# Kernel optimization log

Hardware: AMD Instinct MI355X
Metric: run time of the kernel (lower is better)

## Reference

```python
import jax, jax.numpy as jnp
import numpy as np

B, N, E, H = 2, 2048, 2048, 16
D = E // H  # head_dim = 128


def setup_inputs() -> dict:
    key = jax.random.key(0)
    k1, k2, k3, k4 = jax.random.split(key, 4)
    x = jax.random.normal(k1, (B, N, E), dtype=jnp.float32)
    Wq = jax.random.normal(k2, (E, E), dtype=jnp.float32) * 0.02
    Wkv = jax.random.normal(k3, (2 * E, E), dtype=jnp.float32) * 0.02
    Wout = jax.random.normal(k4, (E, E), dtype=jnp.float32) * 0.02
    return {"x": x, "Wq": Wq, "Wkv": Wkv, "Wout": Wout}


def reference(x, Wq, Wkv, Wout):
    # projections (torch Linear: y = x @ W.T)
    q = x @ Wq.T                      # [b, n, e]
    kv = x @ Wkv.T                    # [b, n, 2e]
    k, v = jnp.split(kv, 2, axis=-1)  # each [b, n, e]

    def split_heads(t):
        return t.reshape(B, N, H, D).transpose(0, 2, 1, 3)  # [b, h, n, d]

    q, k, v = split_heads(q), split_heads(k), split_heads(v)

    scale = D ** -0.5
    sim = jnp.einsum('bhid,bhjd->bhij', q * scale, k)  # [b, h, n, n]

    # causal mask: triu(j - i + 1) masks strictly-future positions
    mask_value = -jnp.finfo(sim.dtype).max
    causal_mask = jnp.triu(jnp.ones((N, N), dtype=bool), k=1)
    sim = jnp.where(causal_mask, mask_value, sim)

    attn = jax.nn.softmax(sim, axis=-1)
    out = jnp.einsum('bhij,bhjd->bhid', attn, v)  # [b, h, n, d]
    out = out.transpose(0, 2, 1, 3).reshape(B, N, E)
    return out @ Wout.T
```

## Files before the change

kernel.cpp:

```cpp
#include <hip/hip_runtime.h>


typedef __bf16 bf16;
typedef bf16 bf16x2 __attribute__((ext_vector_type(2)));
typedef bf16 bf16x4 __attribute__((ext_vector_type(4)));
typedef bf16 bf16x8 __attribute__((ext_vector_type(8)));
typedef float f32x4 __attribute__((ext_vector_type(4)));
typedef float f32x16 __attribute__((ext_vector_type(16)));

typedef const __attribute__((address_space(1))) void cg_void;
typedef __attribute__((address_space(3))) void lds_void;

#define MFMA16(a, b, c) __builtin_amdgcn_mfma_f32_16x16x32_bf16((a), (b), (c), 0, 0, 0)
#define MFMA32(a, b, c) __builtin_amdgcn_mfma_f32_32x32x16_bf16((a), (b), (c), 0, 0, 0)

__device__ __forceinline__ void async_load16(const bf16* g, bf16* l) {
  __builtin_amdgcn_global_load_lds((cg_void*)g, (lds_void*)l, 16, 0, 0);
}

__global__ __launch_bounds__(256) void cast_all_kernel(
    const float* __restrict__ x, const float* __restrict__ wq,
    const float* __restrict__ wkv, const float* __restrict__ wout,
    bf16* __restrict__ xb, bf16* __restrict__ wqkvb, bf16* __restrict__ woutb) {
  long i = (long)blockIdx.x * 256 + threadIdx.x;
  const float* src; bf16* dst; long off;
  if (i < 1048576)      { src = x;    dst = xb;            off = i; }
  else if (i < 2621440) { src = wq;   dst = wqkvb;         off = i - 1048576;
                          if (off >= 524288) { src = wkv; dst = wqkvb + 4194304; off -= 524288; } }
  else                  { src = wout; dst = woutb;         off = i - 2621440; }
  float4 f0 = ((const float4*)src)[2 * off];
  float4 f1 = ((const float4*)src)[2 * off + 1];
  bf16x8 o;
  o[0] = (bf16)f0.x; o[1] = (bf16)f0.y; o[2] = (bf16)f0.z; o[3] = (bf16)f0.w;
  o[4] = (bf16)f1.x; o[5] = (bf16)f1.y; o[6] = (bf16)f1.z; o[7] = (bf16)f1.w;
  ((bf16x8*)dst)[off] = o;
}

#define STAGE_A(bufi, h, tt) do {                              \
    const bf16* g_ = Ag + (h) * 262144 + (tt) * 64;            \
    bf16* d_ = ldsA + (bufi) * 16384 + (h) * 8192;             \
    async_load16(g_, d_);                                      \
    async_load16(g_ + 131072, d_ + 4096);                      \
  } while (0)
#define STAGE_B(bufi, h, tt) do {                              \
    const bf16* g_ = Bg + (h) * 262144 + (tt) * 64;            \
    bf16* d_ = ldsB + (bufi) * 16384 + (h) * 8192;             \
    async_load16(g_, d_);                                      \
    async_load16(g_ + 131072, d_ + 4096);                      \
  } while (0)

__global__ __launch_bounds__(512, 2)
void gemm_qkv_8phase(const bf16* __restrict__ A, const bf16* __restrict__ B,
                     bf16* __restrict__ qk, bf16* __restrict__ vt) {
  __shared__ __attribute__((aligned(16))) bf16 sm[2][2][256][64];
  const int tid = threadIdx.x;
  const int lane = tid & 63;
  const int wid = tid >> 6;
  const int quad = lane >> 4, l15 = lane & 15;
  const int wr = wid >> 2, wc = wid & 3;

  const int lb = (blockIdx.x & 7) * 48 + (blockIdx.x >> 3);
  const int bn = lb % 24, bm = lb / 24;
  const int m0 = bm * 256, n0 = bn * 256;

  const int srow = tid >> 3;
  const int kswz8 = ((tid & 7) ^ (srow & 7)) * 8;
  const bf16* Ag = A + (size_t)(m0 + srow) * 2048 + kswz8;
  const bf16* Bg = B + (size_t)(n0 + srow) * 2048 + kswz8;
  bf16* ldsA = &sm[0][0][0][0] + tid * 8;
  bf16* ldsB = &sm[1][0][0][0] + tid * 8;

  f32x4 acc[8][4];
#pragma unroll
  for (int i = 0; i < 8; ++i)
#pragma unroll
    for (int j = 0; j < 4; ++j) acc[i][j] = {0.f, 0.f, 0.f, 0.f};

  const int r7 = l15 & 7;
  const int arow = (wr * 128 + l15) * 64;
  const int brow = (wc * 64 + l15) * 64;

  STAGE_A(0, 0, 0); STAGE_A(0, 1, 0); STAGE_B(0, 0, 0); STAGE_B(0, 1, 0);
  STAGE_A(1, 0, 1); STAGE_A(1, 1, 1);
  asm volatile("s_waitcnt vmcnt(4)" ::: "memory");
  __builtin_amdgcn_s_barrier();

  for (int t = 0; t < 32; ++t) {
    const int cur = t & 1;
    const bf16* as = &sm[0][0][0][0] + cur * 16384;
    const bf16* bs = &sm[1][0][0][0] + cur * 16384;
#pragma unroll
    for (int ks = 0; ks < 2; ++ks) {
      const int cc = ((ks * 4 + quad) ^ r7) * 8;
      bf16x8 af[8], bfr[4];
#pragma unroll
      for (int i = 0; i < 8; ++i)
        af[i] = *(const bf16x8*)(as + arow + i * 1024 + cc);
#pragma unroll
      for (int j = 0; j < 4; ++j)
        bfr[j] = *(const bf16x8*)(bs + brow + j * 1024 + cc);
      if (t < 31) STAGE_B(1 - cur, ks, t + 1);
      __builtin_amdgcn_s_barrier();
      asm volatile("s_waitcnt lgkmcnt(0)" ::: "memory");
      __builtin_amdgcn_s_setprio(1);
#pragma unroll
      for (int i = 0; i < 8; ++i)
#pragma unroll
        for (int j = 0; j < 4; ++j) acc[i][j] = MFMA16(af[i], bfr[j], acc[i][j]);
      __builtin_amdgcn_s_setprio(0);
      __builtin_amdgcn_s_barrier();
    }
    if (t < 30) {
      STAGE_A(cur, 0, t + 2); STAGE_A(cur, 1, t + 2);
      asm volatile("s_waitcnt vmcnt(4)" ::: "memory");
      __builtin_amdgcn_s_barrier();
    } else if (t == 30) {
      asm volatile("s_waitcnt vmcnt(0)" ::: "memory");
      __builtin_amdgcn_s_barrier();
    }
  }

  if (n0 < 4096) {
#pragma unroll
    for (int i = 0; i < 8; ++i)
#pragma unroll
      for (int r = 0; r < 4; ++r) {
        const size_t base = (size_t)(m0 + wr * 128 + i * 16 + quad * 4 + r) * 4096
                          + n0 + wc * 64 + l15;
#pragma unroll
        for (int j = 0; j < 4; ++j) qk[base + j * 16] = (bf16)acc[i][j][r];
      }
  } else {
    __syncthreads();
    bf16* T = &sm[0][0][0][0];
#pragma unroll
    for (int i = 0; i < 8; ++i)
#pragma unroll
      for (int r = 0; r < 4; ++r) {
        const int nl = wr * 128 + i * 16 + quad * 4 + r;
#pragma unroll
        for (int j = 0; j < 4; ++j) {
          const int fl = wc * 64 + j * 16 + l15;
          T[fl * 256 + ((((nl >> 3) ^ (fl & 31)) << 3) | (nl & 7))] = (bf16)acc[i][j][r];
        }
      }
    __syncthreads();
    const int f0g = n0 - 4096, nb0 = m0 & 2047, b = m0 >> 11;
#pragma unroll
    for (int c = 0; c < 16; ++c) {
      const int idx = c * 512 + tid;
      const int fl = idx >> 5, nb = idx & 31;
      bf16x8 o = *(const bf16x8*)(T + fl * 256 + ((nb ^ (fl & 31)) << 3));
      *(bf16x8*)(vt + (size_t)(b * 2048 + f0g + fl) * 2048 + nb0 + nb * 8) = o;
    }
  }
}

__global__ __launch_bounds__(256, 4)
void gemm_out_kernel(const bf16* __restrict__ A, const bf16* __restrict__ B,
                     float* __restrict__ C, int K, int NN) {
  __shared__ __attribute__((aligned(16))) bf16 smem[8192];
  bf16* As = smem;
  bf16* Bs = smem + 4096;
  const int tid = threadIdx.x;
  const int wave = tid >> 6, lane = tid & 63;
  const int quad = lane >> 4, l15 = lane & 15;
  const int m0 = blockIdx.y * 128, n0 = blockIdx.x * 128;
  const int wm = (wave >> 1) * 64, wn = (wave & 1) * 64;

  f32x4 acc[4][4];
#pragma unroll
  for (int i = 0; i < 4; ++i)
#pragma unroll
    for (int j = 0; j < 4; ++j) acc[i][j] = {0.f, 0.f, 0.f, 0.f};

  const int srow = tid >> 2;
  const int scol = (tid & 3) * 8;
  const bf16* aG = A + (size_t)(m0 + srow) * K + scol;
  const bf16* bG = B + (size_t)(n0 + srow) * K + scol;
  bf16* aL = As + srow * 32 + scol;
  bf16* bL = Bs + srow * 32 + scol;
  const size_t gstep = (size_t)64 * K;

  for (int kt = 0; kt < K; kt += 32) {
    __syncthreads();
    async_load16(aG, aL);
    async_load16(aG + gstep, aL + 64 * 32);
    async_load16(bG, bL);
    async_load16(bG + gstep, bL + 64 * 32);
    aG += 32; bG += 32;
    __syncthreads();

    bf16x8 af[4], bfr[4];
#pragma unroll
    for (int i = 0; i < 4; ++i)
      af[i] = *(const bf16x8*)(As + (wm + i * 16 + l15) * 32 + quad * 8);
#pragma unroll
    for (int j = 0; j < 4; ++j)
      bfr[j] = *(const bf16x8*)(Bs + (wn + j * 16 + l15) * 32 + quad * 8);
#pragma unroll
    for (int i = 0; i < 4; ++i)
#pragma unroll
      for (int j = 0; j < 4; ++j) acc[i][j] = MFMA16(af[i], bfr[j], acc[i][j]);
  }

#pragma unroll
  for (int i = 0; i < 4; ++i) {
#pragma unroll
    for (int r = 0; r < 4; ++r) {
      int row = m0 + wm + i * 16 + quad * 4 + r;
      size_t base = (size_t)row * NN + n0 + wn + l15;
#pragma unroll
      for (int j = 0; j < 4; ++j) C[base + j * 16] = (float)acc[i][j][r];
    }
  }
}

__global__ __launch_bounds__(256, 2)
void attn_kernel(const bf16* __restrict__ qk, const bf16* __restrict__ vt,
                 bf16* __restrict__ yb) {
  constexpr int NSEQ = 2048, E = 2048, QKS = 4096;
  __shared__ __attribute__((aligned(16))) bf16 Ks[2][64 * 128];
  __shared__ __attribute__((aligned(16))) bf16 Vs[2][128 * 64];
  const int tid = threadIdx.x;
  const int wave = tid >> 6, lane = tid & 63;
  const int l31 = lane & 31, half = lane >> 5;
  const int id = blockIdx.x;
  const int slot = (id >> 5) & 15;
  const int bh = (id & 7) | (((id >> 3) & 3) << 3);
  const int b = bh >> 4, h = bh & 15;
  const int qt = (slot < 8) ? slot : 23 - slot;
  const float c1 = 0.08838834764831845f * 1.44269504088896f;

  const int krow_s = tid >> 4, kch_s = tid & 15;
  const int vrow_s = tid >> 3, vch_s = tid & 7;
  const bf16* kg = qk + (size_t)(b * NSEQ) * QKS + 2048 + h * 128;
  const bf16* vg = vt + (size_t)b * E * NSEQ + (size_t)(h * 128) * NSEQ;

  const int diag = 2 * qt + (wave >> 1);
  const int ktmax = 2 * qt + 1;

  {
    bf16* kdst = Ks[0] + tid * 8;
    bf16* vdst = Vs[0] + tid * 8;
#pragma unroll
    for (int p = 0; p < 4; ++p) {
      int r = p * 16 + krow_s;
      async_load16(kg + (size_t)r * QKS + (kch_s ^ (r & 7)) * 8, kdst + p * 2048);
    }
#pragma unroll
    for (int p = 0; p < 4; ++p) {
      int r = p * 32 + vrow_s;
      async_load16(vg + (size_t)r * NSEQ + (vch_s ^ (r & 7)) * 8, vdst + p * 2048);
    }
  }

  const int qrow = qt * 128 + wave * 32 + l31;
  bf16x8 qf[8];
  {
    const bf16* qp = qk + (size_t)(b * NSEQ + qrow) * QKS + h * 128 + half * 8;
#pragma unroll
    for (int k8 = 0; k8 < 8; ++k8) qf[k8] = *(const bf16x8*)(qp + k8 * 16);
  }

  float m = -3.0e38f, l = 0.f;
  f32x16 accO[4];
#pragma unroll
  for (int md = 0; md < 4; ++md)
#pragma unroll
    for (int r = 0; r < 16; ++r) accO[md][r] = 0.f;

  union PU { unsigned u; bf16x2 h; };
  union FU { bf16x8 v; unsigned u[4]; };

  for (int kt = 0; kt <= ktmax; ++kt) {
    const int cur = kt & 1;
    __syncthreads();

    if (kt < ktmax) {
      const int nxt = kt + 1;
      bf16* kdst = Ks[1 - cur] + tid * 8;
      bf16* vdst = Vs[1 - cur] + tid * 8;
#pragma unroll
      for (int p = 0; p < 4; ++p) {
        int r = p * 16 + krow_s;
        async_load16(kg + (size_t)(nxt * 64 + r) * QKS + (kch_s ^ (r & 7)) * 8, kdst + p * 2048);
      }
#pragma unroll
      for (int p = 0; p < 4; ++p) {
        int r = p * 32 + vrow_s;
        async_load16(vg + (size_t)r * NSEQ + nxt * 64 + (vch_s ^ (r & 7)) * 8, vdst + p * 2048);
      }
    }

    if (kt > diag) continue;

    const bf16* ks = Ks[cur];
    const bf16* vs = Vs[cur];

    f32x16 st[2];
#pragma unroll
    for (int mt = 0; mt < 2; ++mt)
#pragma unroll
      for (int r = 0; r < 16; ++r) st[mt][r] = 0.f;
#pragma unroll
    for (int k8 = 0; k8 < 8; ++k8) {
#pragma unroll
      for (int mt = 0; mt < 2; ++mt) {
        int row = mt * 32 + l31;
        int sl = (k8 * 2 + half) ^ (row & 7);
        bf16x8 kf = *(const bf16x8*)(ks + row * 128 + sl * 8);
        st[mt] = MFMA32(kf, qf[k8], st[mt]);
      }
    }

    if (kt == diag) {
#pragma unroll
      for (int mt = 0; mt < 2; ++mt)
#pragma unroll
        for (int r = 0; r < 16; ++r) {
          int t = kt * 64 + mt * 32 + (r & 3) + 8 * (r >> 2) + 4 * half;
          if (t > qrow) st[mt][r] = -3.0e38f;
        }
    }

    float mx = -3.0e38f;
#pragma unroll
    for (int mt = 0; mt < 2; ++mt)
#pragma unroll
      for (int r = 0; r < 16; ++r) mx = fmaxf(mx, st[mt][r]);
    mx = fmaxf(mx, __shfl_xor(mx, 32));
    float mnew = fmaxf(m, mx);
    float alpha = exp2f((m - mnew) * c1);
    float mc = mnew * c1;
    m = mnew;

    float psum = 0.f;
    unsigned pown[2][4][2];
#pragma unroll
    for (int mt = 0; mt < 2; ++mt)
#pragma unroll
      for (int qd = 0; qd < 4; ++qd)
#pragma unroll
        for (int pr = 0; pr < 2; ++pr) {
          float p0 = exp2f(st[mt][qd * 4 + pr * 2] * c1 - mc);
          float p1 = exp2f(st[mt][qd * 4 + pr * 2 + 1] * c1 - mc);
          psum += p0 + p1;
          PU a; a.h[0] = (bf16)p0; a.h[1] = (bf16)p1;
          pown[mt][qd][pr] = a.u;
        }
    psum += __shfl_xor(psum, 32);
    l = l * alpha + psum;

#pragma unroll
    for (int md = 0; md < 4; ++md)
#pragma unroll
      for (int r = 0; r < 16; ++r) accO[md][r] *= alpha;

#pragma unroll
    for (int mt = 0; mt < 2; ++mt)
#pragma unroll
      for (int c = 0; c < 2; ++c) {
        const int qa = 2 * c, qb = 2 * c + 1;
        unsigned ra0 = __shfl_xor(pown[mt][qa][0], 32);
        unsigned ra1 = __shfl_xor(pown[mt][qa][1], 32);
        unsigned rb0 = __shfl_xor(pown[mt][qb][0], 32);
        unsigned rb1 = __shfl_xor(pown[mt][qb][1], 32);
        FU f;
        f.u[0] = half ? rb0 : pown[mt][qa][0];
        f.u[1] = half ? rb1 : pown[mt][qa][1];
        f.u[2] = half ? pown[mt][qb][0] : ra0;
        f.u[3] = half ? pown[mt][qb][1] : ra1;
        const int kk = mt * 2 + c;
#pragma unroll
        for (int md = 0; md < 4; ++md) {
          int row = md * 32 + l31;
          bf16x8 vf = *(const bf16x8*)(vs + row * 64 + (((kk * 2 + half) ^ (row & 7)) * 8));
          accO[md] = MFMA32(vf, f.v, accO[md]);
        }
      }
  }

  float invl = 1.0f / l;
  bf16* yp = yb + (size_t)(b * NSEQ + qrow) * E + h * 128;
#pragma unroll
  for (int md = 0; md < 4; ++md)
#pragma unroll
    for (int rq = 0; rq < 4; ++rq) {
      bf16x4 o;
#pragma unroll
      for (int i = 0; i < 4; ++i) o[i] = (bf16)(accO[md][rq * 4 + i] * invl);
      *(bf16x4*)(yp + md * 32 + rq * 8 + half * 4) = o;
    }
}

extern "C" void kernel_launch(void* const* d_in, const int* in_sizes, int n_in,
                              void* d_out, int out_size, void* d_ws, size_t ws_size,
                              hipStream_t stream) {
  const float* x    = (const float*)d_in[0];
  const float* Wq   = (const float*)d_in[1];
  const float* Wkv  = (const float*)d_in[2];
  const float* Wout = (const float*)d_in[3];
  float* out = (float*)d_out;

  constexpr size_t NX = (size_t)2 * 2048 * 2048;
  constexpr size_t NW = (size_t)2048 * 2048;

  bf16* xb     = (bf16*)d_ws;
  bf16* wqkvb  = xb + NX;
  bf16* woutb  = wqkvb + 3 * NW;
  bf16* qk_b   = woutb + NW;
  bf16* y_b    = qk_b + 2 * NX;
  bf16* vt_b   = y_b + NX;

  cast_all_kernel<<<12288, 256, 0, stream>>>(x, Wq, Wkv, Wout, xb, wqkvb, woutb);

  gemm_qkv_8phase<<<384, 512, 0, stream>>>(xb, wqkvb, qk_b, vt_b);
  attn_kernel<<<512, 256, 0, stream>>>(qk_b, vt_b, y_b);
  gemm_out_kernel<<<dim3(16, 32), 256, 0, stream>>>(y_b, woutb, out, 2048, 2048);
}
```

Measured before the change: 366.6 us.

## Split QKV GEMM into separate QK and V kernels with finer tiles

The fused QKV projection GEMM (384 blocks of 256x256) becomes two kernels. One computes Q/K with 256 blocks and a reworked inner loop that loads A/B fragments in quadrants so LDS reads interleave with MFMA. The other computes V with 256x128 tiles (256 blocks) and the transposed store. The aim is better wave balance across CUs, since 384 blocks gives an uneven tail on 256 CUs, plus more overlap of LDS reads with MFMA. The cost is an extra kernel launch and a second read of the x tiles across the two kernels.

```diff
diff --git a/kernel.cpp b/kernel.cpp
--- a/kernel.cpp
+++ b/kernel.cpp
@@ -48,10 +48,16 @@
     async_load16(g_, d_);                                      \
     async_load16(g_ + 131072, d_ + 4096);                      \
   } while (0)
+#define STAGE_BS(bufi, tt) do {                                \
+    const bf16* g_ = Bg + (tt) * 64;                           \
+    bf16* d_ = ldsB + (bufi) * 8192;                           \
+    async_load16(g_, d_);                                      \
+    async_load16(g_ + 131072, d_ + 4096);                      \
+  } while (0)
 
 __global__ __launch_bounds__(512, 2)
-void gemm_qkv_8phase(const bf16* __restrict__ A, const bf16* __restrict__ B,
-                     bf16* __restrict__ qk, bf16* __restrict__ vt) {
+void gemm_qk_8phase(const bf16* __restrict__ A, const bf16* __restrict__ B,
+                    bf16* __restrict__ qk) {
   __shared__ __attribute__((aligned(16))) bf16 sm[2][2][256][64];
   const int tid = threadIdx.x;
   const int lane = tid & 63;
@@ -59,8 +65,8 @@
   const int quad = lane >> 4, l15 = lane & 15;
   const int wr = wid >> 2, wc = wid & 3;
 
-  const int lb = (blockIdx.x & 7) * 48 + (blockIdx.x >> 3);
-  const int bn = lb % 24, bm = lb / 24;
+  const int lb = (blockIdx.x & 7) * 32 + (blockIdx.x >> 3);
+  const int bm = lb >> 4, bn = lb & 15;
   const int m0 = bm * 256, n0 = bn * 256;
 
   const int srow = tid >> 3;
@@ -77,6 +83,8 @@
     for (int j = 0; j < 4; ++j) acc[i][j] = {0.f, 0.f, 0.f, 0.f};
 
   const int r7 = l15 & 7;
+  const int c0 = (quad ^ r7) * 8;
+  const int c1 = ((4 + quad) ^ r7) * 8;
   const int arow = (wr * 128 + l15) * 64;
   const int brow = (wc * 64 + l15) * 64;
 
@@ -89,27 +97,75 @@
     const int cur = t & 1;
     const bf16* as = &sm[0][0][0][0] + cur * 16384;
     const bf16* bs = &sm[1][0][0][0] + cur * 16384;
-#pragma unroll
-    for (int ks = 0; ks < 2; ++ks) {
-      const int cc = ((ks * 4 + quad) ^ r7) * 8;
-      bf16x8 af[8], bfr[4];
-#pragma unroll
-      for (int i = 0; i < 8; ++i)
-        af[i] = *(const bf16x8*)(as + arow + i * 1024 + cc);
-#pragma unroll
-      for (int j = 0; j < 4; ++j)
-        bfr[j] = *(const bf16x8*)(bs + brow + j * 1024 + cc);
-      if (t < 31) STAGE_B(1 - cur, ks, t + 1);
-      __builtin_amdgcn_s_barrier();
-      asm volatile("s_waitcnt lgkmcnt(0)" ::: "memory");
-      __builtin_amdgcn_s_setprio(1);
-#pragma unroll
-      for (int i = 0; i < 8; ++i)
-#pragma unroll
-        for (int j = 0; j < 4; ++j) acc[i][j] = MFMA16(af[i], bfr[j], acc[i][j]);
-      __builtin_amdgcn_s_setprio(0);
-      __builtin_amdgcn_s_barrier();
-    }
+    bf16x8 a0[4][2], a1[4][2], b0[2][2], b1[2][2];
+
+#pragma unroll
+    for (int i = 0; i < 4; ++i) {
+      a0[i][0] = *(const bf16x8*)(as + arow + i * 1024 + c0);
+      a0[i][1] = *(const bf16x8*)(as + arow + i * 1024 + c1);
+    }
+#pragma unroll
+    for (int j = 0; j < 2; ++j) {
+      b0[j][0] = *(const bf16x8*)(bs + brow + j * 1024 + c0);
+      b0[j][1] = *(const bf16x8*)(bs + brow + j * 1024 + c1);
+    }
+    if (t < 31) STAGE_B(1 - cur, 0, t + 1);
+    asm volatile("s_waitcnt lgkmcnt(8)" ::: "memory");
+    __builtin_amdgcn_s_barrier();
+    asm volatile("s_waitcnt lgkmcnt(0)" ::: "memory");
+    __builtin_amdgcn_s_setprio(1);
+#pragma unroll
+    for (int ks = 0; ks < 2; ++ks)
+#pragma unroll
+      for (int i = 0; i < 4; ++i)
+#pragma unroll
+        for (int j = 0; j < 2; ++j) acc[i][j] = MFMA16(a0[i][ks], b0[j][ks], acc[i][j]);
+    __builtin_amdgcn_s_setprio(0);
+    __builtin_amdgcn_s_barrier();
+
+#pragma unroll
+    for (int j = 0; j < 2; ++j) {
+      b1[j][0] = *(const bf16x8*)(bs + brow + (2 + j) * 1024 + c0);
+      b1[j][1] = *(const bf16x8*)(bs + brow + (2 + j) * 1024 + c1);
+    }
+    if (t < 31) STAGE_B(1 - cur, 1, t + 1);
+    __builtin_amdgcn_s_barrier();
+    asm volatile("s_waitcnt lgkmcnt(0)" ::: "memory");
+    __builtin_amdgcn_s_setprio(1);
+#pragma unroll
+    for (int ks = 0; ks < 2; ++ks)
+#pragma unroll
+      for (int i = 0; i < 4; ++i)
+#pragma unroll
+        for (int j = 0; j < 2; ++j) acc[i][2 + j] = MFMA16(a0[i][ks], b1[j][ks], acc[i][2 + j]);
+    __builtin_amdgcn_s_setprio(0);
+    __builtin_amdgcn_s_barrier();
+
+#pragma unroll
+    for (int i = 0; i < 4; ++i) {
+      a1[i][0] = *(const bf16x8*)(as + arow + (4 + i) * 1024 + c0);
+      a1[i][1] = *(const bf16x8*)(as + arow + (4 + i) * 1024 + c1);
+    }
+    __builtin_amdgcn_s_barrier();
+    asm volatile("s_waitcnt lgkmcnt(0)" ::: "memory");
+    __builtin_amdgcn_s_setprio(1);
+#pragma unroll
+    for (int ks = 0; ks < 2; ++ks)
+#pragma unroll
+      for (int i = 0; i < 4; ++i)
+#pragma unroll
+        for (int j = 0; j < 2; ++j) acc[4 + i][j] = MFMA16(a1[i][ks], b0[j][ks], acc[4 + i][j]);
+    __builtin_amdgcn_s_setprio(0);
+    __builtin_amdgcn_s_barrier();
+
+    __builtin_amdgcn_s_setprio(1);
+#pragma unroll
+    for (int ks = 0; ks < 2; ++ks)
+#pragma unroll
+      for (int i = 0; i < 4; ++i)
+#pragma unroll
+        for (int j = 0; j < 2; ++j) acc[4 + i][2 + j] = MFMA16(a1[i][ks], b1[j][ks], acc[4 + i][2 + j]);
+    __builtin_amdgcn_s_setprio(0);
     if (t < 30) {
       STAGE_A(cur, 0, t + 2); STAGE_A(cur, 1, t + 2);
       asm volatile("s_waitcnt vmcnt(4)" ::: "memory");
@@ -120,39 +176,110 @@
     }
   }
 
-  if (n0 < 4096) {
-#pragma unroll
-    for (int i = 0; i < 8; ++i)
-#pragma unroll
-      for (int r = 0; r < 4; ++r) {
-        const size_t base = (size_t)(m0 + wr * 128 + i * 16 + quad * 4 + r) * 4096
-                          + n0 + wc * 64 + l15;
-#pragma unroll
-        for (int j = 0; j < 4; ++j) qk[base + j * 16] = (bf16)acc[i][j][r];
+#pragma unroll
+  for (int i = 0; i < 8; ++i)
+#pragma unroll
+    for (int r = 0; r < 4; ++r) {
+      const size_t base = (size_t)(m0 + wr * 128 + i * 16 + quad * 4 + r) * 4096
+                        + n0 + wc * 64 + l15;
+#pragma unroll
+      for (int j = 0; j < 4; ++j) qk[base + j * 16] = (bf16)acc[i][j][r];
+    }
+}
+
+__global__ __launch_bounds__(512, 2)
+void gemm_v_8phase(const bf16* __restrict__ A, const bf16* __restrict__ B,
+                   bf16* __restrict__ vt) {
+  __shared__ __attribute__((aligned(16))) bf16 smA[2][256][64];
+  __shared__ __attribute__((aligned(16))) bf16 smB[2][128][64];
+  const int tid = threadIdx.x;
+  const int lane = tid & 63;
+  const int wid = tid >> 6;
+  const int quad = lane >> 4, l15 = lane & 15;
+  const int wr = wid >> 1, wc = wid & 1;
+
+  const int lb = (blockIdx.x & 7) * 32 + (blockIdx.x >> 3);
+  const int bm = lb >> 4, bn = lb & 15;
+  const int m0 = bm * 256, n0 = bn * 128;
+
+  const int srow = tid >> 3;
+  const int kswz8 = ((tid & 7) ^ (srow & 7)) * 8;
+  const bf16* Ag = A + (size_t)(m0 + srow) * 2048 + kswz8;
+  const bf16* Bg = B + (size_t)(n0 + srow) * 2048 + kswz8;
+  bf16* ldsA = &smA[0][0][0] + tid * 8;
+  bf16* ldsB = &smB[0][0][0] + tid * 8;
+
+  f32x4 acc[4][4];
+#pragma unroll
+  for (int i = 0; i < 4; ++i)
+#pragma unroll
+    for (int j = 0; j < 4; ++j) acc[i][j] = {0.f, 0.f, 0.f, 0.f};
+
+  const int r7 = l15 & 7;
+  const int arow = (wr * 64 + l15) * 64;
+  const int brow = (wc * 64 + l15) * 64;
+
+  STAGE_A(0, 0, 0); STAGE_A(0, 1, 0); STAGE_BS(0, 0);
+  STAGE_A(1, 0, 1); STAGE_A(1, 1, 1);
+  asm volatile("s_waitcnt vmcnt(4)" ::: "memory");
+  __builtin_amdgcn_s_barrier();
+
+  for (int t = 0; t < 32; ++t) {
+    const int cur = t & 1;
+    const bf16* as = &smA[0][0][0] + cur * 16384;
+    const bf16* bs = &smB[0][0][0] + cur * 8192;
+#pragma unroll
+    for (int ks = 0; ks < 2; ++ks) {
+      const int cc = ((ks * 4 + quad) ^ r7) * 8;
+      bf16x8 af[4], bfr[4];
+#pragma unroll
+      for (int i = 0; i < 4; ++i)
+        af[i] = *(const bf16x8*)(as + arow + i * 1024 + cc);
+#pragma unroll
+      for (int j = 0; j < 4; ++j)
+        bfr[j] = *(const bf16x8*)(bs + brow + j * 1024 + cc);
+      if (ks == 0 && t < 31) STAGE_BS(1 - cur, t + 1);
+      __builtin_amdgcn_s_barrier();
+      asm volatile("s_waitcnt lgkmcnt(0)" ::: "memory");
+      __builtin_amdgcn_s_setprio(1);
+#pragma unroll
+      for (int i = 0; i < 4; ++i)
+#pragma unroll
+        for (int j = 0; j < 4; ++j) acc[i][j] = MFMA16(af[i], bfr[j], acc[i][j]);
+      __builtin_amdgcn_s_setprio(0);
+      __builtin_amdgcn_s_barrier();
+    }
+    if (t < 30) {
+      STAGE_A(cur, 0, t + 2); STAGE_A(cur, 1, t + 2);
+      asm volatile("s_waitcnt vmcnt(4)" ::: "memory");
+      __builtin_amdgcn_s_barrier();
+    } else if (t == 30) {
+      asm volatile("s_waitcnt vmcnt(0)" ::: "memory");
+      __builtin_amdgcn_s_barrier();
+    }
+  }
+
+  __syncthreads();
+  bf16* T = &smA[0][0][0];
+#pragma unroll
+  for (int i = 0; i < 4; ++i)
+#pragma unroll
+    for (int r = 0; r < 4; ++r) {
+      const int nl = wr * 64 + i * 16 + quad * 4 + r;
+#pragma unroll
+      for (int j = 0; j < 4; ++j) {
+        const int fl = wc * 64 + j * 16 + l15;
+        T[fl * 256 + ((((nl >> 3) ^ (fl & 31)) << 3) | (nl & 7))] = (bf16)acc[i][j][r];
       }
-  } else {
-    __syncthreads();
-    bf16* T = &sm[0][0][0][0];
-#pragma unroll
-    for (int i = 0; i < 8; ++i)
-#pragma unroll
-      for (int r = 0; r < 4; ++r) {
-        const int nl = wr * 128 + i * 16 + quad * 4 + r;
-#pragma unroll
-        for (int j = 0; j < 4; ++j) {
-          const int fl = wc * 64 + j * 16 + l15;
-          T[fl * 256 + ((((nl >> 3) ^ (fl & 31)) << 3) | (nl & 7))] = (bf16)acc[i][j][r];
-        }
-      }
-    __syncthreads();
-    const int f0g = n0 - 4096, nb0 = m0 & 2047, b = m0 >> 11;
-#pragma unroll
-    for (int c = 0; c < 16; ++c) {
-      const int idx = c * 512 + tid;
-      const int fl = idx >> 5, nb = idx & 31;
-      bf16x8 o = *(const bf16x8*)(T + fl * 256 + ((nb ^ (fl & 31)) << 3));
-      *(bf16x8*)(vt + (size_t)(b * 2048 + f0g + fl) * 2048 + nb0 + nb * 8) = o;
-    }
+    }
+  __syncthreads();
+  const int f0g = n0, nb0 = m0 & 2047, b = m0 >> 11;
+#pragma unroll
+  for (int c = 0; c < 8; ++c) {
+    const int idx = c * 512 + tid;
+    const int fl = idx >> 5, nb = idx & 31;
+    bf16x8 o = *(const bf16x8*)(T + fl * 256 + ((nb ^ (fl & 31)) << 3));
+    *(bf16x8*)(vt + (size_t)(b * 2048 + f0g + fl) * 2048 + nb0 + nb * 8) = o;
   }
 }
 
@@ -415,7 +542,8 @@
 
   cast_all_kernel<<<12288, 256, 0, stream>>>(x, Wq, Wkv, Wout, xb, wqkvb, woutb);
 
-  gemm_qkv_8phase<<<384, 512, 0, stream>>>(xb, wqkvb, qk_b, vt_b);
+  gemm_qk_8phase<<<256, 512, 0, stream>>>(xb, wqkvb, qk_b);
+  gemm_v_8phase<<<256, 512, 0, stream>>>(xb, wqkvb + (size_t)4096 * 2048, vt_b);
   attn_kernel<<<512, 256, 0, stream>>>(qk_b, vt_b, y_b);
   gemm_out_kernel<<<dim3(16, 32), 256, 0, stream>>>(y_b, woutb, out, 2048, 2048);
 }
```

Result: faster. 356.3 us (-2.8%).
